# Optimization experiments

Hardware: AMD Instinct MI355X
Metric: run time of the kernel (lower is better)

Reference implementation:

```python
import jax, jax.numpy as jnp
import numpy as np

D_MODEL = 1024
NHEAD = 16
HEAD_DIM = D_MODEL // NHEAD


def setup_inputs() -> dict:
    key = jax.random.key(0)
    ks = jax.random.split(key, 7)
    N, S, E = 2, 2048, D_MODEL
    query = jax.random.normal(ks[0], (N, S, E), dtype=jnp.float32)
    key_t = jax.random.normal(ks[1], (N, S, E), dtype=jnp.float32)
    value = jax.random.normal(ks[2], (N, S, E), dtype=jnp.float32)
    # nn.Linear default init scale ~ 1/sqrt(fan_in)
    s = 1.0 / np.sqrt(E)
    w_in = jax.random.uniform(ks[3], (3 * E, E), jnp.float32, -s, s)
    b_in = jax.random.uniform(ks[4], (3 * E,), jnp.float32, -s, s)
    w_o = jax.random.uniform(ks[5], (E, E), jnp.float32, -s, s)
    b_o = jax.random.uniform(ks[6], (E,), jnp.float32, -s, s)
    return {"query": query, "key": key_t, "value": value,
            "w_in": w_in, "b_in": b_in, "w_o": w_o, "b_o": b_o}


def reference(query, key, value, w_in, b_in, w_o, b_o):
    # NOTE: the torch module computes q,k,v all from `query` (self-attention);
    # the `key`/`value` args are ignored by its forward math.
    N, S, E = query.shape
    H, Dh = NHEAD, HEAD_DIM
    qkv = query @ w_in.T + b_in                      # (N, S, 3E)
    q, k, v = jnp.split(qkv, 3, axis=-1)
    def heads(x):
        return x.reshape(N, S, H, Dh).transpose(0, 2, 1, 3)  # (N, H, S, Dh)
    q, k, v = heads(q), heads(k), heads(v)
    scale = 1.0 / jnp.sqrt(jnp.asarray(Dh, query.dtype))
    scores = jnp.einsum('bhqd,bhkd->bhqk', q, k) * scale     # (N, H, S, S)
    attn = jax.nn.softmax(scores, axis=-1)
    out = jnp.einsum('bhqk,bhkd->bhqd', attn, v)             # (N, H, S, Dh)
    out = out.transpose(0, 2, 1, 3).reshape(N, S, E)
    return out @ w_o.T + b_o
```

## Files before the change

kernel.cpp:

```cpp
#include <hip/hip_runtime.h>
#include <hip/hip_bf16.h>
#include <stdint.h>

#define NB   2
#define SEQ  2048
#define EMB  1024
#define NH   16
#define DH   64
#define MR   (NB*SEQ)
#define E3   (3*EMB)
#define CSC  (0.125f * 1.44269504f)

typedef __attribute__((ext_vector_type(8))) short bf16x8;
typedef __attribute__((ext_vector_type(4))) float f32x4;
typedef __attribute__((ext_vector_type(16))) float f32x16;

__device__ __forceinline__ unsigned short f2bf(float f) {
  unsigned u = __float_as_uint(f);
  unsigned r = (u + 0x7FFF + ((u >> 16) & 1)) >> 16;
  return (unsigned short)r;
}
__device__ __forceinline__ unsigned pack2(float lo, float hi) {
  return (unsigned)f2bf(lo) | ((unsigned)f2bf(hi) << 16);
}
__device__ __forceinline__ float bf2f(unsigned short s) {
  return __uint_as_float(((unsigned)s) << 16);
}
__device__ __forceinline__ unsigned cvtpk(float lo, float hi) {
  unsigned r;
  asm("v_cvt_pk_bf16_f32 %0, %1, %2" : "=v"(r) : "v"(lo), "v"(hi));
  return r;
}

__device__ __forceinline__ void gld16(const unsigned short* g, unsigned short* l) {
  __builtin_amdgcn_global_load_lds(
      (const __attribute__((address_space(1))) unsigned int*)g,
      (__attribute__((address_space(3))) unsigned int*)l,
      16, 0, 0);
}

__global__ void cvt_all(const float* __restrict__ q,
                        const float* __restrict__ w_in,
                        const float* __restrict__ w_o,
                        unsigned short* __restrict__ Xbf,
                        unsigned short* __restrict__ Winbf,
                        unsigned short* __restrict__ Wobf) {
  int b = blockIdx.x;
  const float* src; unsigned short* dst; int off;
  if (b < 2048)      { src = q;    dst = Xbf;   off = b; }
  else if (b < 3584) { src = w_in; dst = Winbf; off = b - 2048; }
  else               { src = w_o;  dst = Wobf;  off = b - 3584; }
  int i = (off * 256 + threadIdx.x) * 8;
  float4 a = *(const float4*)(src + i);
  float4 c = *(const float4*)(src + i + 4);
  uint4 o;
  o.x = pack2(a.x, a.y);
  o.y = pack2(a.z, a.w);
  o.z = pack2(c.x, c.y);
  o.w = pack2(c.z, c.w);
  *(uint4*)(dst + i) = o;
}

template<bool OUT_F32>
__global__ __launch_bounds__(256) void gemm_bt(
    const unsigned short* __restrict__ A,
    const unsigned short* __restrict__ Bt,
    const float* __restrict__ bias,
    void* __restrict__ Cout,
    int K, int ldc, int scale_cols) {
  __shared__ unsigned short As[4096];
  __shared__ unsigned short Bs[4096];
  const int tid  = threadIdx.x;
  const int lane = tid & 63;
  const int w    = tid >> 6;
  const int wm = w >> 1, wn = w & 1;
  const int g = lane >> 4, li = lane & 15;
  const int rowBase = blockIdx.x * 128;
  const int colBase = blockIdx.y * 128;

  f32x4 acc[4][4];
#pragma unroll
  for (int m = 0; m < 4; ++m)
#pragma unroll
    for (int nn = 0; nn < 4; ++nn) { acc[m][nn][0]=0.f; acc[m][nn][1]=0.f; acc[m][nn][2]=0.f; acc[m][nn][3]=0.f; }

  const unsigned short* Ag = A  + (size_t)(rowBase + (tid >> 2)) * K + (tid & 3) * 8;
  const unsigned short* Bg = Bt + (size_t)(colBase + (tid >> 2)) * K + (tid & 3) * 8;

  for (int k0 = 0; k0 < K; k0 += 32) {
    __syncthreads();
    gld16(Ag + k0,                As + tid * 8);
    gld16(Ag + (size_t)64*K + k0, As + 2048 + tid * 8);
    gld16(Bg + k0,                Bs + tid * 8);
    gld16(Bg + (size_t)64*K + k0, Bs + 2048 + tid * 8);
    __syncthreads();

    bf16x8 af[4], bfv[4];
#pragma unroll
    for (int m = 0; m < 4; ++m)
      af[m] = *(const bf16x8*)&As[(wm*64 + m*16 + li) * 32 + g * 8];
#pragma unroll
    for (int nn = 0; nn < 4; ++nn)
      bfv[nn] = *(const bf16x8*)&Bs[(wn*64 + nn*16 + li) * 32 + g * 8];
#pragma unroll
    for (int m = 0; m < 4; ++m)
#pragma unroll
      for (int nn = 0; nn < 4; ++nn)
        acc[m][nn] = __builtin_amdgcn_mfma_f32_16x16x32_bf16(af[m], bfv[nn], acc[m][nn], 0, 0, 0);
  }

#pragma unroll
  for (int nn = 0; nn < 4; ++nn) {
    const int col = colBase + wn*64 + nn*16 + li;
    const float bv = bias[col];
    const float sc = (col < scale_cols) ? CSC : 1.0f;
#pragma unroll
    for (int m = 0; m < 4; ++m) {
      const int r0 = rowBase + wm*64 + m*16 + g*4;
#pragma unroll
      for (int r = 0; r < 4; ++r) {
        float v = (acc[m][nn][r] + bv) * sc;
        if (OUT_F32) ((float*)Cout)[(size_t)(r0 + r) * ldc + col] = v;
        else ((unsigned short*)Cout)[(size_t)(r0 + r) * ldc + col] = f2bf(v);
      }
    }
  }
}

__global__ __launch_bounds__(256, 3) void attn32(
    const unsigned short* __restrict__ qkv,
    unsigned short* __restrict__ O0,
    unsigned short* __restrict__ O1,
    float* __restrict__ ML) {
  __shared__ unsigned short smem[16384];
  char* LB = (char*)smem;

  const int tid  = threadIdx.x;
  const int lane = tid & 63;
  const int w    = tid >> 6;
  const int hi   = lane >> 5;
  const int l31  = lane & 31;
  const int bid  = blockIdx.x;
  const int qb = bid & 15, h = (bid >> 4) & 15, n = (bid >> 8) & 1, z = bid >> 9;
  const size_t rowN = (size_t)n * SEQ;
  const int kt0 = z * 1024;
  const int vp_ = tid & 31, dblk = tid >> 5;
  unsigned short* Oz = z ? O1 : O0;

  bf16x8 qf[4];
  {
    const size_t qr = rowN + qb*128 + w*32 + l31;
#pragma unroll
    for (int kc = 0; kc < 4; ++kc)
      qf[kc] = *(const bf16x8*)&qkv[qr * E3 + h*64 + kc*16 + hi*8];
  }

  f32x16 ZEROV;
#pragma unroll
  for (int i = 0; i < 16; ++i) ZEROV[i] = 0.f;
  f32x16 acc0 = ZEROV, acc1 = ZEROV;
  float ssum[8];
#pragma unroll
  for (int i = 0; i < 8; ++i) ssum[i] = 0.f;

  uint4 pv0, pv1;
  auto stageK = [&](int kt, int buf) {
#pragma unroll
    for (int p = 0; p < 2; ++p) {
      int r = p*32 + (tid >> 3);
      int ch = (tid & 7) ^ (r & 7);
      gld16(&qkv[(rowN + kt + r) * E3 + EMB + h*64 + ch*8],
            &smem[buf*4096 + p*2048 + tid*8]);
    }
  };
  auto loadV = [&](int kt) {
    const unsigned short* vp = &qkv[(rowN + kt + 2*vp_) * E3 + 2*EMB + h*64 + dblk*8];
    pv0 = *(const uint4*)vp;
    pv1 = *(const uint4*)(vp + E3);
  };
  auto writeV = [&](int buf) {
    const unsigned short* s0 = (const unsigned short*)&pv0;
    const unsigned short* s1 = (const unsigned short*)&pv1;
#pragma unroll
    for (int j = 0; j < 8; ++j) {
      int d = dblk*8 + j;
      unsigned val = (unsigned)s0[j] | ((unsigned)s1[j] << 16);
      *(unsigned*)(LB + 16384 + buf*8192 + d*128 + (((vp_>>2) ^ (d&7)) << 4) + (vp_&3)*4) = val;
    }
  };
  auto mkfrag = [&](const float* zz) {
    unsigned a = cvtpk(zz[0], zz[1]);
    unsigned b = cvtpk(zz[2], zz[3]);
    unsigned c = cvtpk(zz[4], zz[5]);
    unsigned d = cvtpk(zz[6], zz[7]);
    unsigned xa = __shfl_xor(a, 32);
    unsigned xb = __shfl_xor(b, 32);
    unsigned xc = __shfl_xor(c, 32);
    unsigned xd = __shfl_xor(d, 32);
    union { bf16x8 v; unsigned u[4]; } r;
    r.u[0] = hi ? xc : a;
    r.u[1] = hi ? xd : b;
    r.u[2] = hi ? c : xa;
    r.u[3] = hi ? d : xb;
    return r.v;
  };

  loadV(kt0);
  stageK(kt0, 0);
  writeV(0);
  __syncthreads();

  for (int t = 0; t < 16; ++t) {
    const int cur = t & 1;
    const bool pre = (t + 1 < 16);
    const int ktn = kt0 + (t + 1) * 64;
    if (pre) { loadV(ktn); stageK(ktn, cur^1); }

    const char* Kb = LB + cur*8192;
    bf16x8 ka[4], kb[4];
#pragma unroll
    for (int kc = 0; kc < 4; ++kc) {
      int ch = kc*2 + hi;
      int sw = (ch ^ (l31 & 7)) << 4;
      ka[kc] = *(const bf16x8*)(Kb + l31*128 + sw);
      kb[kc] = *(const bf16x8*)(Kb + 4096 + l31*128 + sw);
    }
    __builtin_amdgcn_s_setprio(1);
    f32x16 z0 = __builtin_amdgcn_mfma_f32_32x32x16_bf16(ka[0], qf[0], ZEROV, 0, 0, 0);
    f32x16 z1 = __builtin_amdgcn_mfma_f32_32x32x16_bf16(kb[0], qf[0], ZEROV, 0, 0, 0);
#pragma unroll
    for (int kc = 1; kc < 4; ++kc) {
      z0 = __builtin_amdgcn_mfma_f32_32x32x16_bf16(ka[kc], qf[kc], z0, 0, 0, 0);
      z1 = __builtin_amdgcn_mfma_f32_32x32x16_bf16(kb[kc], qf[kc], z1, 0, 0, 0);
    }
    __builtin_amdgcn_s_setprio(0);

#pragma unroll
    for (int i = 0; i < 16; ++i) {
      z0[i] = __builtin_amdgcn_exp2f(z0[i]);
      z1[i] = __builtin_amdgcn_exp2f(z1[i]);
    }
#pragma unroll
    for (int i = 0; i < 8; ++i)
      ssum[i] += (z0[2*i] + z0[2*i+1]) + (z1[2*i] + z1[2*i+1]);

    float zl0[8], zh0[8], zl1[8], zh1[8];
#pragma unroll
    for (int i = 0; i < 8; ++i) { zl0[i] = z0[i]; zh0[i] = z0[i+8]; zl1[i] = z1[i]; zh1[i] = z1[i+8]; }
    bf16x8 pf[4];
    pf[0] = mkfrag(zl0);
    pf[1] = mkfrag(zh0);
    pf[2] = mkfrag(zl1);
    pf[3] = mkfrag(zh1);

    if (pre) writeV(cur ^ 1);

    const char* Vb = LB + 16384 + cur*8192;
    __builtin_amdgcn_s_setprio(1);
#pragma unroll
    for (int c = 0; c < 4; ++c) {
      int ch = c*2 + hi;
      int sw = (ch ^ (l31 & 7)) << 4;
      bf16x8 va = *(const bf16x8*)(Vb + l31*128 + sw);
      bf16x8 vb = *(const bf16x8*)(Vb + 4096 + l31*128 + sw);
      acc0 = __builtin_amdgcn_mfma_f32_32x32x16_bf16(va, pf[c], acc0, 0, 0, 0);
      acc1 = __builtin_amdgcn_mfma_f32_32x32x16_bf16(vb, pf[c], acc1, 0, 0, 0);
    }
    __builtin_amdgcn_s_setprio(0);
    __syncthreads();
  }

#pragma unroll
  for (int st = 4; st; st >>= 1)
#pragma unroll
    for (int i = 0; i < st; ++i) ssum[i] += ssum[i + st];
  float lsum = ssum[0] + __shfl_xor(ssum[0], 32);

  const int qrow_l = w*32 + l31;
  if (hi == 0) {
    size_t grow = rowN + qb*128 + qrow_l;
    ML[(size_t)z*65536 + grow*16 + h] = lsum;
  }

  float rn = 1.0f / lsum;
#pragma unroll
  for (int dt = 0; dt < 2; ++dt) {
#pragma unroll
    for (int r = 0; r < 16; r += 2) {
      float v0 = (dt ? acc1[r]   : acc0[r])   * rn;
      float v1 = (dt ? acc1[r+1] : acc0[r+1]) * rn;
      int d = dt*32 + (r & 3) + 8*(r >> 2) + 4*hi;
      unsigned val = pack2(v0, v1);
      int col32 = d >> 1;
      int g = col32 >> 2;
      *(unsigned*)(LB + qrow_l*128 + ((g ^ (qrow_l & 7)) << 4) + (col32 & 3)*4) = val;
    }
  }
  __syncthreads();
  {
    int row = tid >> 1;
    size_t orow = (rowN + qb*128 + row) * EMB + h*64;
#pragma unroll
    for (int i = 0; i < 4; ++i) {
      int gg = (tid & 1)*4 + i;
      uint4 v = *(const uint4*)(LB + row*128 + ((gg ^ (row & 7)) << 4));
      *(uint4*)&Oz[orow + gg*8] = v;
    }
  }
}

__global__ void attn_combine(const unsigned short* __restrict__ O0,
                             const unsigned short* __restrict__ O1,
                             const float* __restrict__ ML,
                             unsigned short* __restrict__ x2) {
  int idx = (blockIdx.x * 256 + threadIdx.x) * 8;
  int row = idx >> 10;
  int h = (idx & 1023) >> 6;
  float l0 = ML[row*16 + h];
  float l1 = ML[65536 + row*16 + h];
  float rl = 1.0f / (l0 + l1);
  float w0 = l0 * rl, w1 = l1 * rl;
  uint4 u0 = *(const uint4*)(O0 + idx);
  uint4 u1 = *(const uint4*)(O1 + idx);
  const unsigned* p0 = (const unsigned*)&u0;
  const unsigned* p1 = (const unsigned*)&u1;
  uint4 o;
  unsigned* po = (unsigned*)&o;
#pragma unroll
  for (int j = 0; j < 4; ++j) {
    float lo = w0 * bf2f((unsigned short)(p0[j] & 0xFFFF))
             + w1 * bf2f((unsigned short)(p1[j] & 0xFFFF));
    float hv = w0 * bf2f((unsigned short)(p0[j] >> 16))
             + w1 * bf2f((unsigned short)(p1[j] >> 16));
    po[j] = pack2(lo, hv);
  }
  *(uint4*)(x2 + idx) = o;
}

extern "C" void kernel_launch(void* const* d_in, const int* in_sizes, int n_in,
                              void* d_out, int out_size, void* d_ws, size_t ws_size,
                              hipStream_t stream) {
  const float* q    = (const float*)d_in[0];
  const float* w_in = (const float*)d_in[3];
  const float* b_in = (const float*)d_in[4];
  const float* w_o  = (const float*)d_in[5];
  const float* b_o  = (const float*)d_in[6];

  char* ws = (char*)d_ws;
  unsigned short* Wobf  = (unsigned short*)(ws);
  unsigned short* Xbf   = (unsigned short*)(ws + 2097152);
  unsigned short* Winbf = (unsigned short*)(ws + 10485760);
  unsigned short* QKV   = (unsigned short*)(ws + 16777216);
  unsigned short* X2    = (unsigned short*)(ws + 41943040);
  unsigned short* O0    = Xbf;
  unsigned short* O1    = X2;
  float*          ML    = (float*)(ws + 10485760);

  cvt_all<<<4096, 256, 0, stream>>>(q, w_in, w_o, Xbf, Winbf, Wobf);

  gemm_bt<false><<<dim3(32, 24), 256, 0, stream>>>(Xbf, Winbf, b_in, (void*)QKV, EMB, E3, 1024);
  attn32<<<NB * NH * (SEQ / 128) * 2, 256, 0, stream>>>(QKV, O0, O1, ML);
  attn_combine<<<2048, 256, 0, stream>>>(O0, O1, ML, X2);
  gemm_bt<true><<<dim3(32, 8), 256, 0, stream>>>(X2, Wobf, b_o, d_out, EMB, EMB, 0);
}
```

Before: 134.1 us.

## Deepen GEMM K-tile to 64 with swizzled LDS, raise attention occupancy

The projection GEMM now stages a 64-wide K slice per iteration into doubled LDS buffers, using an XOR swizzle on the 16-byte chunk index. This halves the number of barriers per K and is meant to cut LDS bank conflicts on fragment reads. The attention kernel's launch bound goes from 3 to 4 waves per SIMD. Its K-fragment loads are interleaved with the QK MFMAs, and the P fragments are built directly from accumulator elements instead of temporary arrays, to lower register pressure. The tighter register budget risks spills, and the larger LDS footprint may reduce GEMM occupancy.

```diff
diff --git a/kernel.cpp b/kernel.cpp
--- a/kernel.cpp
+++ b/kernel.cpp
@@ -68,8 +68,8 @@
     const float* __restrict__ bias,
     void* __restrict__ Cout,
     int K, int ldc, int scale_cols) {
-  __shared__ unsigned short As[4096];
-  __shared__ unsigned short Bs[4096];
+  __shared__ unsigned short As[8192];
+  __shared__ unsigned short Bs[8192];
   const int tid  = threadIdx.x;
   const int lane = tid & 63;
   const int w    = tid >> 6;
@@ -84,29 +84,37 @@
 #pragma unroll
     for (int nn = 0; nn < 4; ++nn) { acc[m][nn][0]=0.f; acc[m][nn][1]=0.f; acc[m][nn][2]=0.f; acc[m][nn][3]=0.f; }
 
-  const unsigned short* Ag = A  + (size_t)(rowBase + (tid >> 2)) * K + (tid & 3) * 8;
-  const unsigned short* Bg = Bt + (size_t)(colBase + (tid >> 2)) * K + (tid & 3) * 8;
-
-  for (int k0 = 0; k0 < K; k0 += 32) {
+  const int srow = tid >> 3;
+  const int sch  = (tid & 7) ^ (srow & 7);
+  const unsigned short* Ag = A  + (size_t)(rowBase + srow) * K + sch * 8;
+  const unsigned short* Bg = Bt + (size_t)(colBase + srow) * K + sch * 8;
+
+  for (int k0 = 0; k0 < K; k0 += 64) {
     __syncthreads();
-    gld16(Ag + k0,                As + tid * 8);
-    gld16(Ag + (size_t)64*K + k0, As + 2048 + tid * 8);
-    gld16(Bg + k0,                Bs + tid * 8);
-    gld16(Bg + (size_t)64*K + k0, Bs + 2048 + tid * 8);
+#pragma unroll
+    for (int p = 0; p < 4; ++p) {
+      gld16(Ag + (size_t)(p*32)*K + k0, As + p*2048 + tid*8);
+      gld16(Bg + (size_t)(p*32)*K + k0, Bs + p*2048 + tid*8);
+    }
     __syncthreads();
 
-    bf16x8 af[4], bfv[4];
-#pragma unroll
-    for (int m = 0; m < 4; ++m)
-      af[m] = *(const bf16x8*)&As[(wm*64 + m*16 + li) * 32 + g * 8];
-#pragma unroll
-    for (int nn = 0; nn < 4; ++nn)
-      bfv[nn] = *(const bf16x8*)&Bs[(wn*64 + nn*16 + li) * 32 + g * 8];
-#pragma unroll
-    for (int m = 0; m < 4; ++m)
+#pragma unroll
+    for (int kk = 0; kk < 2; ++kk) {
+      const int c = kk*4 + g;
+      const int sw = (c ^ (li & 7)) << 3;
+      bf16x8 af[4], bfv[4];
+#pragma unroll
+      for (int m = 0; m < 4; ++m)
+        af[m] = *(const bf16x8*)&As[(wm*64 + m*16 + li)*64 + sw];
 #pragma unroll
       for (int nn = 0; nn < 4; ++nn)
-        acc[m][nn] = __builtin_amdgcn_mfma_f32_16x16x32_bf16(af[m], bfv[nn], acc[m][nn], 0, 0, 0);
+        bfv[nn] = *(const bf16x8*)&Bs[(wn*64 + nn*16 + li)*64 + sw];
+#pragma unroll
+      for (int m = 0; m < 4; ++m)
+#pragma unroll
+        for (int nn = 0; nn < 4; ++nn)
+          acc[m][nn] = __builtin_amdgcn_mfma_f32_16x16x32_bf16(af[m], bfv[nn], acc[m][nn], 0, 0, 0);
+    }
   }
 
 #pragma unroll
@@ -127,7 +135,7 @@
   }
 }
 
-__global__ __launch_bounds__(256, 3) void attn32(
+__global__ __launch_bounds__(256, 4) void attn32(
     const unsigned short* __restrict__ qkv,
     unsigned short* __restrict__ O0,
     unsigned short* __restrict__ O1,
@@ -188,11 +196,12 @@
       *(unsigned*)(LB + 16384 + buf*8192 + d*128 + (((vp_>>2) ^ (d&7)) << 4) + (vp_&3)*4) = val;
     }
   };
-  auto mkfrag = [&](const float* zz) {
-    unsigned a = cvtpk(zz[0], zz[1]);
-    unsigned b = cvtpk(zz[2], zz[3]);
-    unsigned c = cvtpk(zz[4], zz[5]);
-    unsigned d = cvtpk(zz[6], zz[7]);
+  auto mkfrag = [&](float a0, float a1, float a2, float a3,
+                    float a4, float a5, float a6, float a7) {
+    unsigned a = cvtpk(a0, a1);
+    unsigned b = cvtpk(a2, a3);
+    unsigned c = cvtpk(a4, a5);
+    unsigned d = cvtpk(a6, a7);
     unsigned xa = __shfl_xor(a, 32);
     unsigned xb = __shfl_xor(b, 32);
     unsigned xc = __shfl_xor(c, 32);
@@ -217,21 +226,15 @@
     if (pre) { loadV(ktn); stageK(ktn, cur^1); }
 
     const char* Kb = LB + cur*8192;
-    bf16x8 ka[4], kb[4];
+    __builtin_amdgcn_s_setprio(1);
+    f32x16 z0 = ZEROV, z1 = ZEROV;
 #pragma unroll
     for (int kc = 0; kc < 4; ++kc) {
-      int ch = kc*2 + hi;
-      int sw = (ch ^ (l31 & 7)) << 4;
-      ka[kc] = *(const bf16x8*)(Kb + l31*128 + sw);
-      kb[kc] = *(const bf16x8*)(Kb + 4096 + l31*128 + sw);
-    }
-    __builtin_amdgcn_s_setprio(1);
-    f32x16 z0 = __builtin_amdgcn_mfma_f32_32x32x16_bf16(ka[0], qf[0], ZEROV, 0, 0, 0);
-    f32x16 z1 = __builtin_amdgcn_mfma_f32_32x32x16_bf16(kb[0], qf[0], ZEROV, 0, 0, 0);
-#pragma unroll
-    for (int kc = 1; kc < 4; ++kc) {
-      z0 = __builtin_amdgcn_mfma_f32_32x32x16_bf16(ka[kc], qf[kc], z0, 0, 0, 0);
-      z1 = __builtin_amdgcn_mfma_f32_32x32x16_bf16(kb[kc], qf[kc], z1, 0, 0, 0);
+      const int sw = ((kc*2 + hi) ^ (l31 & 7)) << 4;
+      bf16x8 ka = *(const bf16x8*)(Kb + l31*128 + sw);
+      bf16x8 kb = *(const bf16x8*)(Kb + 4096 + l31*128 + sw);
+      z0 = __builtin_amdgcn_mfma_f32_32x32x16_bf16(ka, qf[kc], z0, 0, 0, 0);
+      z1 = __builtin_amdgcn_mfma_f32_32x32x16_bf16(kb, qf[kc], z1, 0, 0, 0);
     }
     __builtin_amdgcn_s_setprio(0);
 
@@ -244,14 +247,11 @@
     for (int i = 0; i < 8; ++i)
       ssum[i] += (z0[2*i] + z0[2*i+1]) + (z1[2*i] + z1[2*i+1]);
 
-    float zl0[8], zh0[8], zl1[8], zh1[8];
-#pragma unroll
-    for (int i = 0; i < 8; ++i) { zl0[i] = z0[i]; zh0[i] = z0[i+8]; zl1[i] = z1[i]; zh1[i] = z1[i+8]; }
     bf16x8 pf[4];
-    pf[0] = mkfrag(zl0);
-    pf[1] = mkfrag(zh0);
-    pf[2] = mkfrag(zl1);
-    pf[3] = mkfrag(zh1);
+    pf[0] = mkfrag(z0[0], z0[1], z0[2],  z0[3],  z0[4],  z0[5],  z0[6],  z0[7]);
+    pf[1] = mkfrag(z0[8], z0[9], z0[10], z0[11], z0[12], z0[13], z0[14], z0[15]);
+    pf[2] = mkfrag(z1[0], z1[1], z1[2],  z1[3],  z1[4],  z1[5],  z1[6],  z1[7]);
+    pf[3] = mkfrag(z1[8], z1[9], z1[10], z1[11], z1[12], z1[13], z1[14], z1[15]);
 
     if (pre) writeV(cur ^ 1);
 
@@ -259,8 +259,7 @@
     __builtin_amdgcn_s_setprio(1);
 #pragma unroll
     for (int c = 0; c < 4; ++c) {
-      int ch = c*2 + hi;
-      int sw = (ch ^ (l31 & 7)) << 4;
+      const int sw = ((c*2 + hi) ^ (l31 & 7)) << 4;
       bf16x8 va = *(const bf16x8*)(Vb + l31*128 + sw);
       bf16x8 vb = *(const bf16x8*)(Vb + 4096 + l31*128 + sw);
       acc0 = __builtin_amdgcn_mfma_f32_32x32x16_bf16(va, pf[c], acc0, 0, 0, 0);
```

After: 140.9 us. 1.05x slower.
